# Kernel tuning notes

Measured on AMD Instinct MI355X. Metric: run time of the kernel, lower is better.

The kernel has to match this reference:

```python
import jax, jax.numpy as jnp
import numpy as np

V, E, H, B, T, K = 50000, 100, 128, 128, 512, 12
HD = H // 2  # per-direction LSTM hidden = 64
START, STOP = 10, 11


def _lstm_params(k):
    k1, k2, k3, k4 = jax.random.split(k, 4)
    s = 1.0 / np.sqrt(HD)
    return (jax.random.uniform(k1, (4 * HD, E), minval=-s, maxval=s),
            jax.random.uniform(k2, (4 * HD, HD), minval=-s, maxval=s),
            jax.random.uniform(k3, (4 * HD,), minval=-s, maxval=s),
            jax.random.uniform(k4, (4 * HD,), minval=-s, maxval=s))


def setup_inputs() -> dict:
    key = jax.random.key(0)
    ks = jax.random.split(key, 10)
    sentences = jax.random.randint(ks[0], (B, T), 0, V)
    emb = jax.random.normal(ks[1], (V, E)) * 0.1
    Wih_f, Whh_f, bih_f, bhh_f = _lstm_params(ks[2])
    Wih_b, Whh_b, bih_b, bhh_b = _lstm_params(ks[3])
    W_out = jax.random.normal(ks[4], (K, H)) * 0.05
    b_out = jnp.zeros((K,), dtype=jnp.float32)
    transitions = jax.random.normal(ks[5], (K, K))
    transitions = transitions.at[:, START].set(-10000.0).at[STOP, :].set(-10000.0)
    h0 = jax.random.normal(ks[6], (2, B, HD))
    c0 = jax.random.normal(ks[7], (2, B, HD))
    return dict(sentences=sentences, emb=emb,
                Wih_f=Wih_f, Whh_f=Whh_f, bih_f=bih_f, bhh_f=bhh_f,
                Wih_b=Wih_b, Whh_b=Whh_b, bih_b=bih_b, bhh_b=bhh_b,
                W_out=W_out, b_out=b_out, transitions=transitions, h0=h0, c0=c0)


def _lstm_dir(x, h0, c0, Wih, Whh, bih, bhh):
    # x: [T,B,E]; PyTorch gate order i,f,g,o
    def step(carry, xt):
        h, c = carry
        g = xt @ Wih.T + h @ Whh.T + bih + bhh  # [B,4HD]
        i, f, gg, o = jnp.split(g, 4, axis=-1)
        c = jax.nn.sigmoid(f) * c + jax.nn.sigmoid(i) * jnp.tanh(gg)
        h = jax.nn.sigmoid(o) * jnp.tanh(c)
        return (h, c), h
    _, hs = jax.lax.scan(step, (h0, c0), x)
    return hs  # [T,B,HD]


def _viterbi(emis, trans):
    # emis: [T,K]
    def step(prev, em_t):
        v = prev[:, None] + trans          # [K_from, K_to]
        nxt = em_t + jnp.max(v, axis=0)
        return nxt, jnp.argmax(v, axis=0)  # backpointer per to-tag
    last, bps = jax.lax.scan(step, emis[0], emis[1:])  # bps: [T-1,K]
    last_tag = jnp.argmax(last)
    score = jnp.max(last)
    def back(tag, bp):
        prev = bp[tag]
        return prev, prev
    _, head = jax.lax.scan(back, last_tag, bps, reverse=True)  # tags[0..T-2]
    path = jnp.concatenate([head, last_tag[None]])
    return score, path


def reference(sentences, emb, Wih_f, Whh_f, bih_f, bhh_f,
              Wih_b, Whh_b, bih_b, bhh_b, W_out, b_out,
              transitions, h0, c0):
    x = emb[sentences]              # [B,T,E]
    xt = jnp.swapaxes(x, 0, 1)      # [T,B,E]
    hf = _lstm_dir(xt, h0[0], c0[0], Wih_f, Whh_f, bih_f, bhh_f)
    hb = _lstm_dir(xt[::-1], h0[1], c0[1], Wih_b, Whh_b, bih_b, bhh_b)[::-1]
    hcat = jnp.concatenate([hf, hb], axis=-1)      # [T,B,H]
    emis = hcat @ W_out.T + b_out                  # [T,B,K]
    emis = jnp.swapaxes(emis, 0, 1)                # [B,T,K]
    scores, paths = jax.vmap(lambda e: _viterbi(e, transitions))(emis)
    return scores, paths
```

## Files before the change

### kernel.cpp

```cpp
#include <hip/hip_runtime.h>
#include <hip/hip_bf16.h>

#define VV 50000
#define EE 100
#define HD 64
#define BB 128
#define TT 512
#define KK 12

typedef unsigned int uint32;
typedef __bf16 bf16x8 __attribute__((ext_vector_type(8)));
typedef float  f32x4  __attribute__((ext_vector_type(4)));

__device__ __forceinline__ float bf_lo(unsigned u) { return __uint_as_float(u << 16); }
__device__ __forceinline__ float bf_hi(unsigned u) { return __uint_as_float(u & 0xffff0000u); }
__device__ __forceinline__ float rl_f(float v, int lane) {
    return __uint_as_float(__builtin_amdgcn_readlane(__float_as_uint(v), lane));
}
__device__ __forceinline__ float sigm_f(float x) { return 1.f / (1.f + __expf(-x)); }
__device__ __forceinline__ float tanh_f(float x) {
    float e = __expf(2.f * x);
    return 1.f - 2.f / (e + 1.f);
}
__device__ __forceinline__ unsigned short f2bf(float v) {
    return __builtin_bit_cast(unsigned short, __float2bfloat16(v));
}
__device__ __forceinline__ void lds_barrier() {
    asm volatile("s_waitcnt lgkmcnt(0)" ::: "memory");
    __builtin_amdgcn_s_barrier();
    asm volatile("" ::: "memory");
}

#define LDK 136

__global__ __launch_bounds__(256) void k1_mfma(
    const float* __restrict__ emb,
    const float* __restrict__ Wih_f, const float* __restrict__ Wih_b,
    __hip_bfloat16* __restrict__ proj)
{
    __shared__ unsigned short lA[64 * LDK];
    __shared__ unsigned short lB[64 * LDK];

    const int tid = threadIdx.x;
    const int v0  = blockIdx.x * 64;

    for (int i = tid; i < 64 * 20; i += 256) {
        int r = i / 20, c2 = i % 20;
        *(uint32*)&lA[r * LDK + 96 + c2 * 2] = 0u;
        *(uint32*)&lB[r * LDK + 96 + c2 * 2] = 0u;
    }
    {
        const float* asrc = emb + (size_t)v0 * EE;
        const int alim = (VV - v0 < 64 ? VV - v0 : 64) * EE;
        for (int i = tid; i < 64 * EE; i += 256) {
            float v = (i < alim) ? asrc[i] : 0.f;
            lA[(i / EE) * LDK + (i % EE)] = f2bf(v);
        }
    }
    __syncthreads();

    const int w = tid >> 6, l = tid & 63;
    const int lo16 = l & 15, hi = l >> 4;

    bf16x8 afr[4];
    #pragma unroll
    for (int s = 0; s < 4; ++s)
        afr[s] = *(const bf16x8*)&lA[(w * 16 + lo16) * LDK + s * 32 + hi * 8];

    for (int jb = 0; jb < 8; ++jb) {
        const float* Wsrc = ((jb < 4) ? Wih_f : Wih_b) + (size_t)(jb & 3) * 64 * EE;
        __syncthreads();
        for (int i = tid; i < 64 * EE; i += 256)
            lB[(i / EE) * LDK + (i % EE)] = f2bf(Wsrc[i]);
        __syncthreads();

        f32x4 acc[4] = { {0.f,0.f,0.f,0.f}, {0.f,0.f,0.f,0.f},
                         {0.f,0.f,0.f,0.f}, {0.f,0.f,0.f,0.f} };
        #pragma unroll
        for (int s = 0; s < 4; ++s) {
            #pragma unroll
            for (int n = 0; n < 4; ++n) {
                bf16x8 bfr = *(const bf16x8*)&lB[(n * 16 + lo16) * LDK + s * 32 + hi * 8];
                acc[n] = __builtin_amdgcn_mfma_f32_16x16x32_bf16(afr[s], bfr, acc[n], 0, 0, 0);
            }
        }
        #pragma unroll
        for (int n = 0; n < 4; ++n) {
            #pragma unroll
            for (int r = 0; r < 4; ++r) {
                int v = v0 + w * 16 + hi * 4 + r;
                int j = jb * 64 + n * 16 + lo16;
                if (v < VV)
                    proj[(size_t)v * 512 + j] = __float2bfloat16(acc[n][r]);
            }
        }
    }
}

__global__ __launch_bounds__(256, 1) void k2_lstm(
    const int* __restrict__ sent,
    const __hip_bfloat16* __restrict__ proj,
    const float* __restrict__ Whh_f, const float* __restrict__ Whh_b,
    const float* __restrict__ bih_f, const float* __restrict__ bhh_f,
    const float* __restrict__ bih_b, const float* __restrict__ bhh_b,
    const float* __restrict__ h0, const float* __restrict__ c0,
    __hip_bfloat16* __restrict__ Hbuf)
{
    const int b   = blockIdx.x >> 1;
    const int d   = blockIdx.x & 1;
    const int tid = threadIdx.x;
    const int u   = tid & 63;
    const int w   = tid >> 6;

    __shared__ float a_lds[2][256];
    __shared__ __align__(16) float h_lds[4][64];

    const float* Whh = (d == 0 ? Whh_f : Whh_b) + (size_t)tid * HD;
    float wreg[HD];
    #pragma unroll
    for (int k = 0; k < HD / 4; ++k) {
        float4 t = reinterpret_cast<const float4*>(Whh)[k];
        wreg[4*k+0] = t.x; wreg[4*k+1] = t.y; wreg[4*k+2] = t.z; wreg[4*k+3] = t.w;
    }
    const float bias = (d == 0) ? (bih_f[tid] + bhh_f[tid]) : (bih_b[tid] + bhh_b[tid]);

    float h = h0[((size_t)d * BB + b) * HD + u];
    float c = c0[((size_t)d * BB + b) * HD + u];
    h_lds[w][u] = h;

    const int* srow = sent + (size_t)b * TT;
    const int tstep = (d == 0) ? 1 : -1;
    const int t0    = (d == 0) ? 0 : TT - 1;
    const int doff  = d * 256;
    const unsigned short* prj = (const unsigned short*)proj;

    uint32 cur[8], nxt[8];
    #pragma unroll
    for (int i = 0; i < 8; ++i)
        cur[i] = prj[(size_t)srow[t0 + i * tstep] * 512 + doff + tid];

    __hip_bfloat16* hp = Hbuf + ((size_t)t0 * BB + b) * 128 + d * 64 + u;
    const ptrdiff_t hstride = (ptrdiff_t)tstep * BB * 128;

    asm volatile("s_waitcnt lgkmcnt(0)" ::: "memory");

    int pb = 0;
    for (int s0 = 0; s0 < TT; s0 += 8) {
        #pragma unroll
        for (int i = 0; i < 8; ++i) {
            int sn = s0 + 8 + i;
            sn = (sn < TT) ? sn : TT - 1;
            nxt[i] = prj[(size_t)srow[t0 + sn * tstep] * 512 + doff + tid];
        }
        #pragma unroll
        for (int i = 0; i < 8; ++i) {
            const float xp = bf_lo(cur[i]);

            float acc0 = bias + xp, acc1 = 0.f, acc2 = 0.f, acc3 = 0.f;
            #pragma unroll
            for (int k0 = 0; k0 < HD / 4; ++k0) {
                float4 hk = *(const float4*)&h_lds[w][k0 * 4];
                acc0 = fmaf(hk.x, wreg[4*k0 + 0], acc0);
                acc1 = fmaf(hk.y, wreg[4*k0 + 1], acc1);
                acc2 = fmaf(hk.z, wreg[4*k0 + 2], acc2);
                acc3 = fmaf(hk.w, wreg[4*k0 + 3], acc3);
            }
            float g = (acc0 + acc1) + (acc2 + acc3);

            float a = (w == 2) ? tanh_f(g) : sigm_f(g);
            a_lds[pb][tid] = a;
            lds_barrier();
            float ai = a_lds[pb][u];
            float af = a_lds[pb][64 + u];
            float ag = a_lds[pb][128 + u];
            float ao = a_lds[pb][192 + u];
            c = af * c + ai * ag;
            h = ao * tanh_f(c);
            h_lds[w][u] = h;
            pb ^= 1;

            if (tid < 64)
                *hp = __float2bfloat16(h);
            hp += hstride;
        }
        #pragma unroll
        for (int i = 0; i < 8; ++i) cur[i] = nxt[i];
    }
}

__global__ __launch_bounds__(128) void k3_emis(
    const __hip_bfloat16* __restrict__ Hbuf,
    const float* __restrict__ W_out, const float* __restrict__ b_out,
    float* __restrict__ emis)
{
    const int t = blockIdx.x;
    const int b = threadIdx.x;
    __shared__ float Wl[KK * 128];
    __shared__ unsigned short lh[BB * 128];
    for (int i = threadIdx.x; i < KK * 128; i += 128) Wl[i] = W_out[i];

    {
        const uint4* src = reinterpret_cast<const uint4*>(Hbuf + (size_t)t * BB * 128);
        #pragma unroll
        for (int i = 0; i < 16; ++i) {
            int e = i * 128 + b;
            uint4 v = src[e];
            int r = e >> 4, s = e & 15;
            *(uint4*)((char*)lh + r * 256 + ((s * 16) ^ ((r & 15) << 4))) = v;
        }
    }
    __syncthreads();

    float acc[KK];
    #pragma unroll
    for (int k = 0; k < KK; ++k) acc[k] = b_out[k];

    #pragma unroll
    for (int s = 0; s < 16; ++s) {
        uint4 hv = *(const uint4*)((const char*)lh + b * 256 + ((s * 16) ^ ((b & 15) << 4)));
        float hf[8];
        hf[0] = bf_lo(hv.x); hf[1] = bf_hi(hv.x);
        hf[2] = bf_lo(hv.y); hf[3] = bf_hi(hv.y);
        hf[4] = bf_lo(hv.z); hf[5] = bf_hi(hv.z);
        hf[6] = bf_lo(hv.w); hf[7] = bf_hi(hv.w);
        #pragma unroll
        for (int k = 0; k < KK; ++k) {
            #pragma unroll
            for (int r = 0; r < 8; ++r)
                acc[k] = fmaf(hf[r], Wl[k * 128 + s * 8 + r], acc[k]);
        }
    }
    float* e = emis + ((size_t)b * TT + t) * KK;
    #pragma unroll
    for (int k = 0; k < KK; k += 4) {
        float4 v = make_float4(acc[k], acc[k+1], acc[k+2], acc[k+3]);
        *reinterpret_cast<float4*>(e + k) = v;
    }
}

__global__ __launch_bounds__(64) void k4_viterbi(
    const float* __restrict__ emis, const float* __restrict__ trans,
    float* __restrict__ out)
{
    const int b    = blockIdx.x;
    const int lane = threadIdx.x;
    __shared__ float em_lds[TT * KK];
    __shared__ unsigned char bp[(TT - 1) * KK + 4];

    {
        const uint4* e4 = reinterpret_cast<const uint4*>(emis + (size_t)b * TT * KK);
        uint4* l4 = reinterpret_cast<uint4*>(em_lds);
        for (int i = lane; i < TT * KK / 4; i += 64) l4[i] = e4[i];
    }
    __syncthreads();

    const int jj = (lane < KK) ? lane : 0;
    float tc[KK];
    #pragma unroll
    for (int i = 0; i < KK; ++i) tc[i] = trans[i * KK + jj];

    float vj = em_lds[jj];
    float sv[KK];
    #pragma unroll
    for (int i = 0; i < KK; ++i) sv[i] = rl_f(vj, i);

    for (int t = 1; t < TT; ++t) {
        float best = sv[0] + tc[0];
        int bi = 0;
        #pragma unroll
        for (int i = 1; i < KK; ++i) {
            float cnd = sv[i] + tc[i];
            bool gt = cnd > best;
            best = gt ? cnd : best;
            bi   = gt ? i : bi;
        }
        if (lane < KK) bp[(t - 1) * KK + lane] = (unsigned char)bi;
        vj = best + em_lds[t * KK + jj];
        #pragma unroll
        for (int i = 0; i < KK; ++i) sv[i] = rl_f(vj, i);
    }

    float best = sv[0]; int bt = 0;
    #pragma unroll
    for (int i = 1; i < KK; ++i) { if (sv[i] > best) { best = sv[i]; bt = i; } }

    if (lane == 0) {
        out[b] = best;
        float* path = out + BB + (size_t)b * TT;
        int tag = bt;
        path[TT - 1] = (float)tag;
        for (int t = TT - 2; t >= 0; --t) {
            tag = bp[t * KK + tag];
            path[t] = (float)tag;
        }
    }
}

extern "C" void kernel_launch(void* const* d_in, const int* in_sizes, int n_in,
                              void* d_out, int out_size, void* d_ws, size_t ws_size,
                              hipStream_t stream) {
    const int*   sent  = (const int*)  d_in[0];
    const float* emb   = (const float*)d_in[1];
    const float* Wih_f = (const float*)d_in[2];
    const float* Whh_f = (const float*)d_in[3];
    const float* bih_f = (const float*)d_in[4];
    const float* bhh_f = (const float*)d_in[5];
    const float* Wih_b = (const float*)d_in[6];
    const float* Whh_b = (const float*)d_in[7];
    const float* bih_b = (const float*)d_in[8];
    const float* bhh_b = (const float*)d_in[9];
    const float* W_out = (const float*)d_in[10];
    const float* b_out = (const float*)d_in[11];
    const float* trans = (const float*)d_in[12];
    const float* h0    = (const float*)d_in[13];
    const float* c0    = (const float*)d_in[14];
    float* out = (float*)d_out;

    char* ws = (char*)d_ws;
    __hip_bfloat16* proj = (__hip_bfloat16*)ws;
    size_t off = (((size_t)VV * 512 * 2) + 255) & ~(size_t)255;
    __hip_bfloat16* Hbuf = (__hip_bfloat16*)(ws + off);
    off += (((size_t)TT * BB * 128 * 2) + 255) & ~(size_t)255;
    float* emis = (float*)(ws + off);

    k1_mfma<<<dim3((VV + 63) / 64), 256, 0, stream>>>(emb, Wih_f, Wih_b, proj);
    k2_lstm<<<dim3(2 * BB), 256, 0, stream>>>(sent, proj, Whh_f, Whh_b,
                                              bih_f, bhh_f, bih_b, bhh_b,
                                              h0, c0, Hbuf);
    k3_emis<<<dim3(TT), 128, 0, stream>>>(Hbuf, W_out, b_out, emis);
    k4_viterbi<<<dim3(BB), 64, 0, stream>>>(emis, trans, out);
}
```

Before: 570.1 us.

## Fuse both LSTM directions per block with fp16 dot2 and register-prefetched Wih tiles

The LSTM kernel now runs forward and backward directions in one block per batch row. It keeps both recurrent weight sets as packed fp16 in registers, builds the h vector with DPP plus cvt_pkrtz, broadcasts it through readlane, and accumulates with fdot2. This removes the h LDS round trip and gives two independent dependency chains per step, which hide latency while halving the grid. Separately, the input-projection kernel prefetches the next weight tile into registers while running MFMA on the current one. The cost is lower precision in the recurrence (fp16 weights and h), a larger register footprint, and fewer blocks on the device.

```diff
diff --git a/kernel.cpp b/kernel.cpp
--- a/kernel.cpp
+++ b/kernel.cpp
@@ -11,6 +11,7 @@
 typedef unsigned int uint32;
 typedef __bf16 bf16x8 __attribute__((ext_vector_type(8)));
 typedef float  f32x4  __attribute__((ext_vector_type(4)));
+typedef _Float16 half2v __attribute__((ext_vector_type(2)));
 
 __device__ __forceinline__ float bf_lo(unsigned u) { return __uint_as_float(u << 16); }
 __device__ __forceinline__ float bf_hi(unsigned u) { return __uint_as_float(u & 0xffff0000u); }
@@ -24,6 +25,14 @@
 }
 __device__ __forceinline__ unsigned short f2bf(float v) {
     return __builtin_bit_cast(unsigned short, __float2bfloat16(v));
+}
+__device__ __forceinline__ float fdot2(half2v a, uint32 bbits, float c) {
+    half2v bv = __builtin_bit_cast(half2v, bbits);
+#if __has_builtin(__builtin_amdgcn_fdot2)
+    return __builtin_amdgcn_fdot2(a, bv, c, false);
+#else
+    return c + (float)a[0] * (float)bv[0] + (float)a[1] * (float)bv[1];
+#endif
 }
 __device__ __forceinline__ void lds_barrier() {
     asm volatile("s_waitcnt lgkmcnt(0)" ::: "memory");
@@ -57,6 +66,14 @@
             lA[(i / EE) * LDK + (i % EE)] = f2bf(v);
         }
     }
+    {
+        const float* W0 = Wih_f;
+        #pragma unroll
+        for (int i = 0; i < 25; ++i) {
+            int idx = i * 256 + tid;
+            lB[(idx / EE) * LDK + (idx % EE)] = f2bf(W0[idx]);
+        }
+    }
     __syncthreads();
 
     const int w = tid >> 6, l = tid & 63;
@@ -68,11 +85,12 @@
         afr[s] = *(const bf16x8*)&lA[(w * 16 + lo16) * LDK + s * 32 + hi * 8];
 
     for (int jb = 0; jb < 8; ++jb) {
-        const float* Wsrc = ((jb < 4) ? Wih_f : Wih_b) + (size_t)(jb & 3) * 64 * EE;
-        __syncthreads();
-        for (int i = tid; i < 64 * EE; i += 256)
-            lB[(i / EE) * LDK + (i % EE)] = f2bf(Wsrc[i]);
-        __syncthreads();
+        float nb[25];
+        if (jb < 7) {
+            const float* Wn = ((jb + 1 < 4) ? Wih_f : Wih_b) + (size_t)((jb + 1) & 3) * 64 * EE;
+            #pragma unroll
+            for (int i = 0; i < 25; ++i) nb[i] = Wn[i * 256 + tid];
+        }
 
         f32x4 acc[4] = { {0.f,0.f,0.f,0.f}, {0.f,0.f,0.f,0.f},
                          {0.f,0.f,0.f,0.f}, {0.f,0.f,0.f,0.f} };
@@ -93,6 +111,15 @@
                 if (v < VV)
                     proj[(size_t)v * 512 + j] = __float2bfloat16(acc[n][r]);
             }
+        }
+        if (jb < 7) {
+            __syncthreads();
+            #pragma unroll
+            for (int i = 0; i < 25; ++i) {
+                int idx = i * 256 + tid;
+                lB[(idx / EE) * LDK + (idx % EE)] = f2bf(nb[i]);
+            }
+            __syncthreads();
         }
     }
 }
@@ -106,85 +133,102 @@
     const float* __restrict__ h0, const float* __restrict__ c0,
     __hip_bfloat16* __restrict__ Hbuf)
 {
-    const int b   = blockIdx.x >> 1;
-    const int d   = blockIdx.x & 1;
+    const int b   = blockIdx.x;
     const int tid = threadIdx.x;
     const int u   = tid & 63;
     const int w   = tid >> 6;
 
-    __shared__ float a_lds[2][256];
-    __shared__ __align__(16) float h_lds[4][64];
-
-    const float* Whh = (d == 0 ? Whh_f : Whh_b) + (size_t)tid * HD;
-    float wreg[HD];
-    #pragma unroll
-    for (int k = 0; k < HD / 4; ++k) {
-        float4 t = reinterpret_cast<const float4*>(Whh)[k];
-        wreg[4*k+0] = t.x; wreg[4*k+1] = t.y; wreg[4*k+2] = t.z; wreg[4*k+3] = t.w;
-    }
-    const float bias = (d == 0) ? (bih_f[tid] + bhh_f[tid]) : (bih_b[tid] + bhh_b[tid]);
-
-    float h = h0[((size_t)d * BB + b) * HD + u];
-    float c = c0[((size_t)d * BB + b) * HD + u];
-    h_lds[w][u] = h;
+    __shared__ float a_lds[2][2][256];
+
+    half2v wA[32], wB[32];
+    {
+        const float* rA = Whh_f + (size_t)tid * HD;
+        const float* rB = Whh_b + (size_t)tid * HD;
+        #pragma unroll
+        for (int p = 0; p < 16; ++p) {
+            float4 a4 = reinterpret_cast<const float4*>(rA)[p];
+            float4 b4 = reinterpret_cast<const float4*>(rB)[p];
+            wA[2*p]   = half2v{(_Float16)a4.x, (_Float16)a4.y};
+            wA[2*p+1] = half2v{(_Float16)a4.z, (_Float16)a4.w};
+            wB[2*p]   = half2v{(_Float16)b4.x, (_Float16)b4.y};
+            wB[2*p+1] = half2v{(_Float16)b4.z, (_Float16)b4.w};
+        }
+    }
+    const float biasA = bih_f[tid] + bhh_f[tid];
+    const float biasB = bih_b[tid] + bhh_b[tid];
+
+    float hA = h0[((size_t)0 * BB + b) * HD + u];
+    float cA = c0[((size_t)0 * BB + b) * HD + u];
+    float hB = h0[((size_t)1 * BB + b) * HD + u];
+    float cB = c0[((size_t)1 * BB + b) * HD + u];
 
     const int* srow = sent + (size_t)b * TT;
-    const int tstep = (d == 0) ? 1 : -1;
-    const int t0    = (d == 0) ? 0 : TT - 1;
-    const int doff  = d * 256;
     const unsigned short* prj = (const unsigned short*)proj;
 
-    uint32 cur[8], nxt[8];
-    #pragma unroll
-    for (int i = 0; i < 8; ++i)
-        cur[i] = prj[(size_t)srow[t0 + i * tstep] * 512 + doff + tid];
-
-    __hip_bfloat16* hp = Hbuf + ((size_t)t0 * BB + b) * 128 + d * 64 + u;
-    const ptrdiff_t hstride = (ptrdiff_t)tstep * BB * 128;
-
-    asm volatile("s_waitcnt lgkmcnt(0)" ::: "memory");
+    uint32 curA[4], curB[4], nxtA[4], nxtB[4];
+    #pragma unroll
+    for (int i = 0; i < 4; ++i) {
+        curA[i] = prj[(size_t)srow[i] * 512 + tid];
+        curB[i] = prj[(size_t)srow[TT - 1 - i] * 512 + 256 + tid];
+    }
+
+    __hip_bfloat16* hpA = Hbuf + ((size_t)0 * BB + b) * 128 + u;
+    __hip_bfloat16* hpB = Hbuf + ((size_t)(TT - 1) * BB + b) * 128 + 64 + u;
+    const ptrdiff_t hstride = (ptrdiff_t)BB * 128;
 
     int pb = 0;
-    for (int s0 = 0; s0 < TT; s0 += 8) {
-        #pragma unroll
-        for (int i = 0; i < 8; ++i) {
-            int sn = s0 + 8 + i;
+    for (int s0 = 0; s0 < TT; s0 += 4) {
+        #pragma unroll
+        for (int i = 0; i < 4; ++i) {
+            int sn = s0 + 4 + i;
             sn = (sn < TT) ? sn : TT - 1;
-            nxt[i] = prj[(size_t)srow[t0 + sn * tstep] * 512 + doff + tid];
-        }
-        #pragma unroll
-        for (int i = 0; i < 8; ++i) {
-            const float xp = bf_lo(cur[i]);
-
-            float acc0 = bias + xp, acc1 = 0.f, acc2 = 0.f, acc3 = 0.f;
-            #pragma unroll
-            for (int k0 = 0; k0 < HD / 4; ++k0) {
-                float4 hk = *(const float4*)&h_lds[w][k0 * 4];
-                acc0 = fmaf(hk.x, wreg[4*k0 + 0], acc0);
-                acc1 = fmaf(hk.y, wreg[4*k0 + 1], acc1);
-                acc2 = fmaf(hk.z, wreg[4*k0 + 2], acc2);
-                acc3 = fmaf(hk.w, wreg[4*k0 + 3], acc3);
+            nxtA[i] = prj[(size_t)srow[sn] * 512 + tid];
+            nxtB[i] = prj[(size_t)srow[TT - 1 - sn] * 512 + 256 + tid];
+        }
+        #pragma unroll
+        for (int i = 0; i < 4; ++i) {
+            int dA = __builtin_amdgcn_update_dpp(0, __float_as_int(hA), 0xB1, 0xF, 0xF, false);
+            int dB = __builtin_amdgcn_update_dpp(0, __float_as_int(hB), 0xB1, 0xF, 0xF, false);
+            uint32 hbA = __builtin_bit_cast(uint32,
+                __builtin_amdgcn_cvt_pkrtz(hA, __int_as_float(dA)));
+            uint32 hbB = __builtin_bit_cast(uint32,
+                __builtin_amdgcn_cvt_pkrtz(hB, __int_as_float(dB)));
+
+            float aA0 = biasA + bf_lo(curA[i]), aA1 = 0.f;
+            float aB0 = biasB + bf_lo(curB[i]), aB1 = 0.f;
+            #pragma unroll
+            for (int q = 0; q < 32; q += 2) {
+                uint32 sA0 = (uint32)__builtin_amdgcn_readlane((int)hbA, 2 * q);
+                uint32 sA1 = (uint32)__builtin_amdgcn_readlane((int)hbA, 2 * q + 2);
+                uint32 sB0 = (uint32)__builtin_amdgcn_readlane((int)hbB, 2 * q);
+                uint32 sB1 = (uint32)__builtin_amdgcn_readlane((int)hbB, 2 * q + 2);
+                aA0 = fdot2(wA[q],     sA0, aA0);
+                aA1 = fdot2(wA[q + 1], sA1, aA1);
+                aB0 = fdot2(wB[q],     sB0, aB0);
+                aB1 = fdot2(wB[q + 1], sB1, aB1);
             }
-            float g = (acc0 + acc1) + (acc2 + acc3);
-
-            float a = (w == 2) ? tanh_f(g) : sigm_f(g);
-            a_lds[pb][tid] = a;
+            float gA = aA0 + aA1, gB = aB0 + aB1;
+
+            float actA = (w == 2) ? tanh_f(gA) : sigm_f(gA);
+            float actB = (w == 2) ? tanh_f(gB) : sigm_f(gB);
+            a_lds[pb][0][tid] = actA;
+            a_lds[pb][1][tid] = actB;
             lds_barrier();
-            float ai = a_lds[pb][u];
-            float af = a_lds[pb][64 + u];
-            float ag = a_lds[pb][128 + u];
-            float ao = a_lds[pb][192 + u];
-            c = af * c + ai * ag;
-            h = ao * tanh_f(c);
-            h_lds[w][u] = h;
+            float iA = a_lds[pb][0][u],       fA = a_lds[pb][0][64 + u];
+            float ggA = a_lds[pb][0][128 + u], oA = a_lds[pb][0][192 + u];
+            float iB = a_lds[pb][1][u],       fB = a_lds[pb][1][64 + u];
+            float ggB = a_lds[pb][1][128 + u], oB = a_lds[pb][1][192 + u];
+            cA = fA * cA + iA * ggA;  hA = oA * tanh_f(cA);
+            cB = fB * cB + iB * ggB;  hB = oB * tanh_f(cB);
             pb ^= 1;
 
-            if (tid < 64)
-                *hp = __float2bfloat16(h);
-            hp += hstride;
-        }
-        #pragma unroll
-        for (int i = 0; i < 8; ++i) cur[i] = nxt[i];
+            if (w == 0) *hpA = __float2bfloat16(hA);
+            if (w == 1) *hpB = __float2bfloat16(hB);
+            hpA += hstride;
+            hpB -= hstride;
+        }
+        #pragma unroll
+        for (int i = 0; i < 4; ++i) { curA[i] = nxtA[i]; curB[i] = nxtB[i]; }
     }
 }
 
@@ -324,9 +368,9 @@
     float* emis = (float*)(ws + off);
 
     k1_mfma<<<dim3((VV + 63) / 64), 256, 0, stream>>>(emb, Wih_f, Wih_b, proj);
-    k2_lstm<<<dim3(2 * BB), 256, 0, stream>>>(sent, proj, Whh_f, Whh_b,
-                                              bih_f, bhh_f, bih_b, bhh_b,
-                                              h0, c0, Hbuf);
+    k2_lstm<<<dim3(BB), 256, 0, stream>>>(sent, proj, Whh_f, Whh_b,
+                                          bih_f, bhh_f, bih_b, bhh_b,
+                                          h0, c0, Hbuf);
     k3_emis<<<dim3(TT), 128, 0, stream>>>(Hbuf, W_out, b_out, emis);
     k4_viterbi<<<dim3(BB), 64, 0, stream>>>(emis, trans, out);
 }
```

Result: slower. 606.4 us (+6.4%).
